# Optimization experiments

Hardware: AMD Instinct MI355X
Metric: run time of the kernel (lower is better)

## Reference

```python
import jax, jax.numpy as jnp
import numpy as np

PAD, CLS, SEP, UNK = 0, 1, 2, 3
VOCAB, DIM, LATENT = 30000, 768, 5000
B, L, C = 16, 1024, 8


def setup_inputs() -> dict:
    key = jax.random.key(0)
    k1, k2, k3 = jax.random.split(key, 3)
    x = jax.random.randint(k1, (B, L, C), 0, VOCAB, dtype=jnp.int64)
    char_emb = jax.random.normal(k2, (VOCAB, DIM), dtype=jnp.float32)
    latent_mat = jax.random.normal(k3, (LATENT, DIM), dtype=jnp.float32) * (LATENT ** -0.5)
    return {"x": x, "char_emb": char_emb, "latent_mat": latent_mat}


def reference(x, char_emb, latent_mat):
    b, l, c = x.shape
    chars = x.reshape(-1, c)                       # (N, C)
    embs = char_emb[chars]                         # (N, C, D) gather
    pad_mask = chars == PAD                        # (N, C)
    embs = jnp.where(pad_mask[..., None], 0.0, embs)
    summed = embs.sum(axis=1)                      # (N, D)
    counts = jnp.clip((~pad_mask).sum(axis=-1), 1, None)  # (N,)
    lang_emb = jnp.tanh(summed / counts[:, None].astype(summed.dtype))  # (N, D)

    # soft codebook attention: matmul -> softmax -> matmul
    scores = jnp.einsum('nd,kd->nk', lang_emb, latent_mat)   # (N, LATENT)
    dist = jax.nn.softmax(scores, axis=-1)
    latent_emb = jnp.einsum('nk,kd->nd', dist, latent_mat)    # (N, D)
    sde = lang_emb + latent_emb

    # special-token overwrite based on first char id
    first = chars[:, 0]
    for tid in (PAD, UNK, SEP, CLS):
        sde = jnp.where((first == tid)[:, None], char_emb[tid], sde)
    return sde.reshape(b, l, -1)
```

## Files before the change

kernel.cpp:

```cpp
#include <hip/hip_runtime.h>

#define PAD_ID 0
#define NTOK   16384
#define DIM    768
#define KLAT   5000
#define KPAD   5024
#define NSTEP  157
#define TILE_SH 24576

typedef float f32x4 __attribute__((ext_vector_type(4)));
typedef __bf16 bf16x8 __attribute__((ext_vector_type(8)));

__device__ __forceinline__ unsigned short f2bf(float f) {
    unsigned int u = __float_as_uint(f);
    u += 0x7fffu + ((u >> 16) & 1u);
    return (unsigned short)(u >> 16);
}
__device__ __forceinline__ float bf2f(unsigned short h) {
    return __uint_as_float(((unsigned int)h) << 16);
}
__device__ __forceinline__ void async_cp16(const unsigned short* g, unsigned short* l) {
    __builtin_amdgcn_global_load_lds(
        (const __attribute__((address_space(1))) unsigned int*)g,
        (__attribute__((address_space(3))) unsigned int*)l, 16, 0, 0);
}

__global__ __launch_bounds__(256) void cvt_latS(const float* __restrict__ latent,
                                                unsigned short* __restrict__ latbS) {
    int g = blockIdx.x * 256 + threadIdx.x;
    if (g >= NSTEP * 24 * 2 * 64) return;
    int lane = g & 63; int rest = g >> 6;
    int h = rest & 1;  int kfr = rest >> 1;
    int kf = kfr % 24; int t  = kfr / 24;
    int row = t * 32 + h * 16 + (lane & 15);
    int col = kf * 32 + (lane >> 4) * 8;
    float4 v0 = make_float4(0.f,0.f,0.f,0.f), v1 = v0;
    if (row < KLAT) {
        v0 = *(const float4*)(latent + (long)row * DIM + col);
        v1 = *(const float4*)(latent + (long)row * DIM + col + 4);
    }
    uint4 o;
    o.x = (unsigned)f2bf(v0.x) | ((unsigned)f2bf(v0.y) << 16);
    o.y = (unsigned)f2bf(v0.z) | ((unsigned)f2bf(v0.w) << 16);
    o.z = (unsigned)f2bf(v1.x) | ((unsigned)f2bf(v1.y) << 16);
    o.w = (unsigned)f2bf(v1.z) | ((unsigned)f2bf(v1.w) << 16);
    *(uint4*)(latbS + (size_t)g * 8) = o;
}

__global__ __launch_bounds__(256) void cvt_latT(const float* __restrict__ latent,
                                                unsigned short* __restrict__ latbT) {
    int g = blockIdx.x * 256 + threadIdx.x;
    if (g >= NSTEP * DIM * 4) return;
    int kk8 = g & 3; int rest = g >> 2;
    int d = rest % DIM; int t = rest / DIM;
    int kk0 = kk8 * 8;
    unsigned short v[8];
    #pragma unroll
    for (int j = 0; j < 8; ++j) {
        int row = t * 32 + kk0 + j;
        v[j] = (row < KLAT) ? f2bf(latent[(long)row * DIM + d]) : (unsigned short)0;
    }
    *(uint4*)(latbT + (size_t)g * 8) = *(uint4*)v;
}

__global__ __launch_bounds__(192) void build_lang(const int* __restrict__ x,
                                                  const float* __restrict__ cemb,
                                                  unsigned short* __restrict__ langb) {
    int tok = blockIdx.x;
    int t = threadIdx.x;
    const int* xs = x + tok * 8;
    int ids[8]; int cnt = 0;
    #pragma unroll
    for (int c = 0; c < 8; ++c) { ids[c] = xs[c]; cnt += (ids[c] != PAD_ID); }
    float4 acc = make_float4(0.f, 0.f, 0.f, 0.f);
    #pragma unroll
    for (int c = 0; c < 8; ++c) {
        if (ids[c] != PAD_ID) {
            float4 v = *(const float4*)(cemb + (long)ids[c] * DIM + t * 4);
            acc.x += v.x; acc.y += v.y; acc.z += v.z; acc.w += v.w;
        }
    }
    float cntf = (float)max(cnt, 1);
    unsigned int u0 = (unsigned int)f2bf(tanhf(acc.x / cntf)) |
                      ((unsigned int)f2bf(tanhf(acc.y / cntf)) << 16);
    unsigned int u1 = (unsigned int)f2bf(tanhf(acc.z / cntf)) |
                      ((unsigned int)f2bf(tanhf(acc.w / cntf)) << 16);
    *(uint2*)(langb + tok * DIM + t * 4) = make_uint2(u0, u1);
}

__global__ __launch_bounds__(256, 1) void fused_sde(
        const int* __restrict__ x, const float* __restrict__ cemb,
        const unsigned short* __restrict__ langb,
        const unsigned short* __restrict__ latbS,
        const unsigned short* __restrict__ latbT,
        float* __restrict__ out) {
    __shared__ unsigned short sLat[TILE_SH];
    __shared__ unsigned short sP[64 * 40];
    __shared__ float sL[64];

    const int tid  = threadIdx.x;
    const int w    = tid >> 6;
    const int lane = tid & 63;
    const int ln   = lane & 15;
    const int quad = lane >> 4;
    const int m0   = blockIdx.x * 64;

    uint4 qf[24];
    {
        const unsigned short* qr = langb + (m0 + w * 16 + ln) * DIM;
        #pragma unroll
        for (int kf = 0; kf < 24; ++kf)
            qf[kf] = *(const uint4*)(qr + kf * 32 + quad * 8);
    }

    f32x4 accO[4][12];
    #pragma unroll
    for (int mt = 0; mt < 4; ++mt)
        #pragma unroll
        for (int dt = 0; dt < 12; ++dt)
            accO[mt][dt] = (f32x4){0.f, 0.f, 0.f, 0.f};
    float lpart = 0.f;

    #pragma unroll
    for (int i = 0; i < 12; ++i)
        async_cp16(latbS + ((size_t)i * 256 + tid) * 8,
                   sLat + (i * 256 + (tid & ~63)) * 8);
    __syncthreads();

    for (int s = 0; s < NSTEP; ++s) {
        uint4 bO[12];
        {
            const unsigned short* bt = latbT + (size_t)s * TILE_SH;
            #pragma unroll
            for (int dt = 0; dt < 12; ++dt)
                bO[dt] = *(const uint4*)(bt + (w * 192 + dt * 16 + ln) * 32 + quad * 8);
        }

        f32x4 s0 = {0.f,0.f,0.f,0.f}, s1 = {0.f,0.f,0.f,0.f};
        #pragma unroll
        for (int kf = 0; kf < 24; ++kf) {
            bf16x8 a0 = *(const bf16x8*)&sLat[(kf * 128 + lane) * 8];
            bf16x8 a1 = *(const bf16x8*)&sLat[(kf * 128 + 64 + lane) * 8];
            bf16x8 b  = *(const bf16x8*)&qf[kf];
            s0 = __builtin_amdgcn_mfma_f32_16x16x32_bf16(a0, b, s0, 0, 0, 0);
            s1 = __builtin_amdgcn_mfma_f32_16x16x32_bf16(a1, b, s1, 0, 0, 0);
        }

        {
            const int k0 = s * 32;
            unsigned short* prow = &sP[(w * 16 + ln) * 40];
            #pragma unroll
            for (int r = 0; r < 4; ++r) {
                int lat0 = k0 + quad * 4 + r;
                float e0 = (lat0 < KLAT) ? __expf(s0[r]) : 0.f;
                float e1 = (lat0 + 16 < KLAT) ? __expf(s1[r]) : 0.f;
                lpart += e0 + e1;
                prow[quad * 4 + r]      = f2bf(e0);
                prow[16 + quad * 4 + r] = f2bf(e1);
            }
        }
        __syncthreads();

        {
            int nt = (s + 1 < NSTEP) ? s + 1 : 0;
            const unsigned short* gs = latbS + (size_t)nt * TILE_SH;
            #pragma unroll
            for (int i = 0; i < 12; ++i)
                async_cp16(gs + (i * 256 + tid) * 8,
                           sLat + (i * 256 + (tid & ~63)) * 8);
        }

        bf16x8 pA[4];
        #pragma unroll
        for (int mt = 0; mt < 4; ++mt)
            pA[mt] = *(const bf16x8*)&sP[(mt * 16 + ln) * 40 + quad * 8];
        #pragma unroll
        for (int dt = 0; dt < 12; ++dt) {
            bf16x8 b = *(const bf16x8*)&bO[dt];
            #pragma unroll
            for (int mt = 0; mt < 4; ++mt)
                accO[mt][dt] = __builtin_amdgcn_mfma_f32_16x16x32_bf16(
                    pA[mt], b, accO[mt][dt], 0, 0, 0);
        }
        __syncthreads();
    }

    lpart += __shfl_xor(lpart, 16, 64);
    lpart += __shfl_xor(lpart, 32, 64);
    if (lane < 16) sL[w * 16 + lane] = lpart;
    __syncthreads();

    #pragma unroll
    for (int mt = 0; mt < 4; ++mt) {
        int tl0 = mt * 16 + quad * 4;
        float linv[4]; int fid[4];
        #pragma unroll
        for (int r = 0; r < 4; ++r) {
            linv[r] = 1.0f / sL[tl0 + r];
            fid[r]  = x[(m0 + tl0 + r) * 8];
        }
        #pragma unroll
        for (int dt = 0; dt < 12; ++dt) {
            int d = w * 192 + dt * 16 + ln;
            #pragma unroll
            for (int r = 0; r < 4; ++r) {
                int tok = m0 + tl0 + r;
                float v = accO[mt][dt][r] * linv[r] + bf2f(langb[tok * DIM + d]);
                if (fid[r] < 4) v = cemb[fid[r] * DIM + d];
                out[tok * DIM + d] = v;
            }
        }
    }
}

extern "C" void kernel_launch(void* const* d_in, const int* in_sizes, int n_in,
                              void* d_out, int out_size, void* d_ws, size_t ws_size,
                              hipStream_t stream) {
    const int*   x      = (const int*)d_in[0];
    const float* cemb   = (const float*)d_in[1];
    const float* latent = (const float*)d_in[2];
    float* out = (float*)d_out;

    unsigned short* langb = (unsigned short*)d_ws;
    unsigned short* latbS = langb + (size_t)NTOK * DIM;
    unsigned short* latbT = latbS + (size_t)NSTEP * TILE_SH;

    int nS = NSTEP * 24 * 2 * 64;
    int nT = NSTEP * DIM * 4;
    cvt_latS<<<(nS + 255) / 256, 256, 0, stream>>>(latent, latbS);
    cvt_latT<<<(nT + 255) / 256, 256, 0, stream>>>(latent, latbT);
    build_lang<<<NTOK, 192, 0, stream>>>(x, cemb, langb);
    fused_sde<<<NTOK / 64, 256, 0, stream>>>(x, cemb, langb, latbS, latbT, out);
}
```

Measured before the change: 582.4 us.

## Halve tokens per block and split score GEMM across warps for occupancy

Shrinks the fused block from 64 to 32 tokens, doubling the grid to 512 blocks and allowing two blocks per CU via launch bounds. Each warp now computes scores for one 16-token group and one half of the 32-latent step, instead of redundantly covering all latents for its own token group. The row sums are reduced across the two latent halves in the epilogue. The latbT loads are split into three staggered batches interleaved with compute to hide global latency. Each block now streams the whole latent matrix for half as many tokens, doubling total latent traffic in exchange for more parallelism and lower register pressure.

```diff
diff --git a/kernel.cpp b/kernel.cpp
--- a/kernel.cpp
+++ b/kernel.cpp
@@ -7,6 +7,7 @@
 #define KPAD   5024
 #define NSTEP  157
 #define TILE_SH 24576
+#define TOKB   32
 
 typedef float f32x4 __attribute__((ext_vector_type(4)));
 typedef __bf16 bf16x8 __attribute__((ext_vector_type(8)));
@@ -88,34 +89,36 @@
     *(uint2*)(langb + tok * DIM + t * 4) = make_uint2(u0, u1);
 }
 
-__global__ __launch_bounds__(256, 1) void fused_sde(
+__global__ __launch_bounds__(256, 2) void fused_sde(
         const int* __restrict__ x, const float* __restrict__ cemb,
         const unsigned short* __restrict__ langb,
         const unsigned short* __restrict__ latbS,
         const unsigned short* __restrict__ latbT,
         float* __restrict__ out) {
     __shared__ unsigned short sLat[TILE_SH];
-    __shared__ unsigned short sP[64 * 40];
-    __shared__ float sL[64];
+    __shared__ unsigned short sP[TOKB * 40];
+    __shared__ float sL[2][TOKB];
 
     const int tid  = threadIdx.x;
     const int w    = tid >> 6;
     const int lane = tid & 63;
     const int ln   = lane & 15;
     const int quad = lane >> 4;
-    const int m0   = blockIdx.x * 64;
+    const int tt   = w & 1;
+    const int lt   = w >> 1;
+    const int m0   = blockIdx.x * TOKB;
 
     uint4 qf[24];
     {
-        const unsigned short* qr = langb + (m0 + w * 16 + ln) * DIM;
+        const unsigned short* qr = langb + (m0 + tt * 16 + ln) * DIM;
         #pragma unroll
         for (int kf = 0; kf < 24; ++kf)
             qf[kf] = *(const uint4*)(qr + kf * 32 + quad * 8);
     }
 
-    f32x4 accO[4][12];
-    #pragma unroll
-    for (int mt = 0; mt < 4; ++mt)
+    f32x4 accO[2][12];
+    #pragma unroll
+    for (int mt = 0; mt < 2; ++mt)
         #pragma unroll
         for (int dt = 0; dt < 12; ++dt)
             accO[mt][dt] = (f32x4){0.f, 0.f, 0.f, 0.f};
@@ -127,39 +130,54 @@
                    sLat + (i * 256 + (tid & ~63)) * 8);
     __syncthreads();
 
+    const int aBase = lt * 64 + lane;
+    const int bBase = (w * 192 + ln) * 32 + quad * 8;
+
     for (int s = 0; s < NSTEP; ++s) {
-        uint4 bO[12];
+        const unsigned short* bt = latbT + (size_t)s * TILE_SH;
+
+        uint4 bO0[4];
+        #pragma unroll
+        for (int dt = 0; dt < 4; ++dt)
+            bO0[dt] = *(const uint4*)(bt + bBase + dt * 512);
+
+        f32x4 sva = {0.f,0.f,0.f,0.f}, svb = {0.f,0.f,0.f,0.f};
+        #pragma unroll
+        for (int kp = 0; kp < 12; ++kp) {
+            bf16x8 a0 = *(const bf16x8*)&sLat[((2 * kp)     * 128 + aBase) * 8];
+            bf16x8 a1 = *(const bf16x8*)&sLat[((2 * kp + 1) * 128 + aBase) * 8];
+            bf16x8 b0 = *(const bf16x8*)&qf[2 * kp];
+            bf16x8 b1 = *(const bf16x8*)&qf[2 * kp + 1];
+            sva = __builtin_amdgcn_mfma_f32_16x16x32_bf16(a0, b0, sva, 0, 0, 0);
+            svb = __builtin_amdgcn_mfma_f32_16x16x32_bf16(a1, b1, svb, 0, 0, 0);
+        }
+
+        uint4 bO1[4];
+        #pragma unroll
+        for (int dt = 0; dt < 4; ++dt)
+            bO1[dt] = *(const uint4*)(bt + bBase + (dt + 4) * 512);
+
         {
-            const unsigned short* bt = latbT + (size_t)s * TILE_SH;
-            #pragma unroll
-            for (int dt = 0; dt < 12; ++dt)
-                bO[dt] = *(const uint4*)(bt + (w * 192 + dt * 16 + ln) * 32 + quad * 8);
-        }
-
-        f32x4 s0 = {0.f,0.f,0.f,0.f}, s1 = {0.f,0.f,0.f,0.f};
-        #pragma unroll
-        for (int kf = 0; kf < 24; ++kf) {
-            bf16x8 a0 = *(const bf16x8*)&sLat[(kf * 128 + lane) * 8];
-            bf16x8 a1 = *(const bf16x8*)&sLat[(kf * 128 + 64 + lane) * 8];
-            bf16x8 b  = *(const bf16x8*)&qf[kf];
-            s0 = __builtin_amdgcn_mfma_f32_16x16x32_bf16(a0, b, s0, 0, 0, 0);
-            s1 = __builtin_amdgcn_mfma_f32_16x16x32_bf16(a1, b, s1, 0, 0, 0);
-        }
-
-        {
-            const int k0 = s * 32;
-            unsigned short* prow = &sP[(w * 16 + ln) * 40];
-            #pragma unroll
-            for (int r = 0; r < 4; ++r) {
-                int lat0 = k0 + quad * 4 + r;
-                float e0 = (lat0 < KLAT) ? __expf(s0[r]) : 0.f;
-                float e1 = (lat0 + 16 < KLAT) ? __expf(s1[r]) : 0.f;
-                lpart += e0 + e1;
-                prow[quad * 4 + r]      = f2bf(e0);
-                prow[16 + quad * 4 + r] = f2bf(e1);
-            }
+            const int lat0 = s * 32 + lt * 16 + quad * 4;
+            f32x4 sv = sva + svb;
+            float e0 = (lat0     < KLAT) ? __expf(sv[0]) : 0.f;
+            float e1 = (lat0 + 1 < KLAT) ? __expf(sv[1]) : 0.f;
+            float e2 = (lat0 + 2 < KLAT) ? __expf(sv[2]) : 0.f;
+            float e3 = (lat0 + 3 < KLAT) ? __expf(sv[3]) : 0.f;
+            lpart += (e0 + e1) + (e2 + e3);
+            unsigned int p01 = (unsigned)f2bf(e0) | ((unsigned)f2bf(e1) << 16);
+            unsigned int p23 = (unsigned)f2bf(e2) | ((unsigned)f2bf(e3) << 16);
+            *(uint2*)&sP[(tt * 16 + ln) * 40 + lt * 16 + quad * 4] =
+                make_uint2(p01, p23);
         }
         __syncthreads();
+
+        bf16x8 pA0 = *(const bf16x8*)&sP[ln * 40 + quad * 8];
+        bf16x8 pA1 = *(const bf16x8*)&sP[(16 + ln) * 40 + quad * 8];
+        uint4 bO2[4];
+        #pragma unroll
+        for (int dt = 0; dt < 4; ++dt)
+            bO2[dt] = *(const uint4*)(bt + bBase + (dt + 8) * 512);
 
         {
             int nt = (s + 1 < NSTEP) ? s + 1 : 0;
@@ -170,33 +188,39 @@
                            sLat + (i * 256 + (tid & ~63)) * 8);
         }
 
-        bf16x8 pA[4];
-        #pragma unroll
-        for (int mt = 0; mt < 4; ++mt)
-            pA[mt] = *(const bf16x8*)&sP[(mt * 16 + ln) * 40 + quad * 8];
-        #pragma unroll
-        for (int dt = 0; dt < 12; ++dt) {
-            bf16x8 b = *(const bf16x8*)&bO[dt];
-            #pragma unroll
-            for (int mt = 0; mt < 4; ++mt)
-                accO[mt][dt] = __builtin_amdgcn_mfma_f32_16x16x32_bf16(
-                    pA[mt], b, accO[mt][dt], 0, 0, 0);
+        #pragma unroll
+        for (int dt = 0; dt < 4; ++dt) {
+            bf16x8 b = *(const bf16x8*)&bO0[dt];
+            accO[0][dt] = __builtin_amdgcn_mfma_f32_16x16x32_bf16(pA0, b, accO[0][dt], 0, 0, 0);
+            accO[1][dt] = __builtin_amdgcn_mfma_f32_16x16x32_bf16(pA1, b, accO[1][dt], 0, 0, 0);
+        }
+        #pragma unroll
+        for (int dt = 0; dt < 4; ++dt) {
+            bf16x8 b = *(const bf16x8*)&bO1[dt];
+            accO[0][dt + 4] = __builtin_amdgcn_mfma_f32_16x16x32_bf16(pA0, b, accO[0][dt + 4], 0, 0, 0);
+            accO[1][dt + 4] = __builtin_amdgcn_mfma_f32_16x16x32_bf16(pA1, b, accO[1][dt + 4], 0, 0, 0);
+        }
+        #pragma unroll
+        for (int dt = 0; dt < 4; ++dt) {
+            bf16x8 b = *(const bf16x8*)&bO2[dt];
+            accO[0][dt + 8] = __builtin_amdgcn_mfma_f32_16x16x32_bf16(pA0, b, accO[0][dt + 8], 0, 0, 0);
+            accO[1][dt + 8] = __builtin_amdgcn_mfma_f32_16x16x32_bf16(pA1, b, accO[1][dt + 8], 0, 0, 0);
         }
         __syncthreads();
     }
 
     lpart += __shfl_xor(lpart, 16, 64);
     lpart += __shfl_xor(lpart, 32, 64);
-    if (lane < 16) sL[w * 16 + lane] = lpart;
+    if (lane < 16) sL[lt][tt * 16 + lane] = lpart;
     __syncthreads();
 
     #pragma unroll
-    for (int mt = 0; mt < 4; ++mt) {
+    for (int mt = 0; mt < 2; ++mt) {
         int tl0 = mt * 16 + quad * 4;
         float linv[4]; int fid[4];
         #pragma unroll
         for (int r = 0; r < 4; ++r) {
-            linv[r] = 1.0f / sL[tl0 + r];
+            linv[r] = 1.0f / (sL[0][tl0 + r] + sL[1][tl0 + r]);
             fid[r]  = x[(m0 + tl0 + r) * 8];
         }
         #pragma unroll
@@ -230,5 +254,5 @@
     cvt_latS<<<(nS + 255) / 256, 256, 0, stream>>>(latent, latbS);
     cvt_latT<<<(nT + 255) / 256, 256, 0, stream>>>(latent, latbT);
     build_lang<<<NTOK, 192, 0, stream>>>(x, cemb, langb);
-    fused_sde<<<NTOK / 64, 256, 0, stream>>>(x, cemb, langb, latbS, latbT, out);
-}
+    fused_sde<<<NTOK / TOKB, 256, 0, stream>>>(x, cemb, langb, latbS, latbT, out);
+}
```

After: 590.3 us. No clear change (+1.4%).
